# Performance work log

Measured on AMD Instinct MI355X. Metric: run time of the kernel, lower is better.

Reference implementation:

```python
import jax, jax.numpy as jnp
import numpy as np

INPUT_SIZE = 512
LABEL_NUM = 8
OUTPUT_SIZE = 64
H1 = 1024  # shared bottom width
H2 = 512   # expert hidden width
B = 8192


def setup_inputs() -> dict:
    key = jax.random.key(0)
    ks = jax.random.split(key, 8)
    s_in = 1.0 / np.sqrt(INPUT_SIZE)
    s_h1 = 1.0 / np.sqrt(H1)
    s_h2 = 1.0 / np.sqrt(H2)
    return {
        "input": jax.random.normal(ks[0], (B, INPUT_SIZE), dtype=jnp.float32),
        "category": jax.random.randint(ks[1], (B,), 0, LABEL_NUM, dtype=jnp.int32),
        # shared bottom Linear(input_size, 1024): stored as [in, out]
        "W_in": jax.random.uniform(ks[2], (INPUT_SIZE, H1), jnp.float32, -s_in, s_in),
        "b_in": jax.random.uniform(ks[3], (H1,), jnp.float32, -s_in, s_in),
        # per-expert Linear(1024, 512) stacked over experts
        "W1": jax.random.uniform(ks[4], (LABEL_NUM, H1, H2), jnp.float32, -s_h1, s_h1),
        "b1": jax.random.uniform(ks[5], (LABEL_NUM, H2), jnp.float32, -s_h1, s_h1),
        # per-expert Linear(512, output_size) stacked over experts
        "W2": jax.random.uniform(ks[6], (LABEL_NUM, H2, OUTPUT_SIZE), jnp.float32, -s_h2, s_h2),
        "b2": jax.random.uniform(ks[7], (LABEL_NUM, OUTPUT_SIZE), jnp.float32, -s_h2, s_h2),
    }


def reference(input, category, W_in, b_in, W1, b1, W2, b2):
    # Shared bottom: Linear + ELU -> [B, H1]
    mid = jax.nn.elu(input @ W_in + b_in)
    # Run all experts densely, then hard-select per-sample expert output.
    # (Faithful to per-sample hard routing; small expert count makes this clean.)
    h = jax.nn.elu(jnp.einsum("bd,edh->beh", mid, W1) + b1[None, :, :])  # [B,E,H2]
    out_all = jnp.einsum("beh,eho->beo", h, W2) + b2[None, :, :]          # [B,E,O]
    # gather the chosen expert's output for each sample
    out = jnp.take_along_axis(out_all, category[:, None, None].astype(jnp.int32).repeat(1, axis=1), axis=1)
    return out[:, 0, :]  # [B, O]
```

## Files before the change

### kernel.cpp

```cpp
#include <hip/hip_runtime.h>

typedef unsigned short u16;
typedef unsigned int u32;
typedef __bf16 bf16x8 __attribute__((ext_vector_type(8)));
typedef float f32x4 __attribute__((ext_vector_type(4)));

#define GLD_LDS(gptr, lptr) \
  __builtin_amdgcn_global_load_lds((const __attribute__((address_space(1))) void*)(gptr), \
                                   (__attribute__((address_space(3))) void*)(lptr), 16, 0, 0)

__device__ __forceinline__ u16 f2b(float f) {
  union { __bf16 h; u16 u; } v; v.h = (__bf16)f; return v.u;
}
__device__ __forceinline__ float elu1(float v) {
  return v > 0.f ? v : (__expf(v) - 1.f);
}

__device__ void transpose_tile(float (*tbuf)[65], const float* __restrict__ src,
                               u16* __restrict__ dst, int R, int C, int tr, int tc,
                               size_t zoff) {
  const int tid = threadIdx.x;
  const float* sp = src + zoff + (size_t)(tr * 64) * C + tc * 64;
#pragma unroll
  for (int i = 0; i < 4; i++) {
    const int rr = (tid >> 4) + i * 16, f = tid & 15;
    float4 v = *reinterpret_cast<const float4*>(sp + (size_t)rr * C + f * 4);
    tbuf[rr][f * 4 + 0] = v.x; tbuf[rr][f * 4 + 1] = v.y;
    tbuf[rr][f * 4 + 2] = v.z; tbuf[rr][f * 4 + 3] = v.w;
  }
  __syncthreads();
  u16* dp = dst + zoff + (size_t)(tc * 64) * R + tr * 64;
#pragma unroll
  for (int i = 0; i < 4; i++) {
    const int u = tid + i * 256;
    const int c = u >> 4, rq = u & 15;
    ushort4 w;
    w.x = f2b(tbuf[rq * 4 + 0][c]); w.y = f2b(tbuf[rq * 4 + 1][c]);
    w.z = f2b(tbuf[rq * 4 + 2][c]); w.w = f2b(tbuf[rq * 4 + 3][c]);
    *reinterpret_cast<ushort4*>(dp + (size_t)c * R + rq * 4) = w;
  }
}

__device__ void hist_body(int rb, const int* __restrict__ cat, int* __restrict__ cnts) {
  __shared__ int c8[8];
  const int tid = threadIdx.x;
  if (tid < 8) c8[tid] = 0;
  __syncthreads();
  if (tid < 128) atomicAdd(&c8[cat[rb * 128 + tid]], 1);
  __syncthreads();
  if (tid < 8) cnts[rb * 8 + tid] = c8[tid];
}

__device__ void scatter_body(int rb, const int* __restrict__ cat,
                             const int* __restrict__ cnts,
                             int* __restrict__ list, int* __restrict__ off) {
  __shared__ int lc[512];
  __shared__ int lcur[8];
  __shared__ int starts[8];
  const int tid = threadIdx.x;
  lc[tid] = cnts[tid];
  lc[tid + 256] = cnts[tid + 256];
  if (tid < 8) lcur[tid] = 0;
  __syncthreads();
  if (tid < 8) {
    const int c = tid;
    int base = 0;
    for (int cc = 0; cc < c; cc++) {
      int s = 0;
      for (int b = 0; b < 64; b++) s += lc[b * 8 + cc];
      base += s;
    }
    int pre = 0;
    for (int b = 0; b < rb; b++) pre += lc[b * 8 + c];
    starts[c] = base + pre;
    if (rb == 0) {
      off[c] = base;
      if (c == 7) {
        int s = 0;
        for (int b = 0; b < 64; b++) s += lc[b * 8 + 7];
        off[8] = base + s;
      }
    }
  }
  __syncthreads();
  if (tid < 128) {
    const int idx = rb * 128 + tid;
    const int c = cat[idx];
    const int r = atomicAdd(&lcur[c], 1);
    list[starts[c] + r] = idx;
  }
}

__global__ __launch_bounds__(256) void wsmall(const float* __restrict__ W_in,
                                              const int* __restrict__ cat,
                                              u16* __restrict__ o0, int* __restrict__ cnts) {
  __shared__ float tbuf[64][65];
  if (blockIdx.x >= 128) { hist_body(blockIdx.x - 128, cat, cnts); return; }
  transpose_tile(tbuf, W_in, o0, 512, 1024, blockIdx.x >> 4, blockIdx.x & 15, 0);
}


template<int LAYER, int BN, int K, int N>
__global__ __launch_bounds__(256, 4) void gemm_t(
    const float* __restrict__ Xf, const u16* __restrict__ A,
    const u16* __restrict__ Bw, const float* __restrict__ bias,
    const int* __restrict__ list, const int* __restrict__ off,
    u16* __restrict__ outb, float* __restrict__ outf,
    const int* __restrict__ cat, const int* __restrict__ cnts,
    int* __restrict__ wlist, int* __restrict__ woff,
    const float* __restrict__ Wc1, const float* __restrict__ Wc2,
    u16* __restrict__ o1, u16* __restrict__ o2) {
  struct GBuf { alignas(16) u16 As[2][2048]; alignas(16) u16 Bs[2][BN * 32]; };
  __shared__ union SM { GBuf g; float tbuf[64][65]; } sm;

  const int tid = threadIdx.x;

  if constexpr (LAYER == 1) {
    if (blockIdx.y == 8) {
      if (blockIdx.x < 64) scatter_body(blockIdx.x, cat, cnts, wlist, woff);
      return;
    }
    if (blockIdx.y >= 9) {
      if (blockIdx.y <= 16) {
        const int t = (blockIdx.y - 9) * 128 + blockIdx.x;
        const int z = t >> 7, rem = t & 127;
        transpose_tile(sm.tbuf, Wc1, o1, 1024, 512, rem >> 3, rem & 7,
                       (size_t)z * 1024 * 512);
      } else if (blockIdx.x < 64) {
        const int t = blockIdx.x, z = t >> 3;
        transpose_tile(sm.tbuf, Wc2, o2, 512, 64, t & 7, 0, (size_t)z * 512 * 64);
      }
      return;
    }
  }

  int tidx, col0;
  if constexpr (LAYER == 1) {
    const int orig = blockIdx.y * 128 + blockIdx.x;
    const int work = (orig & 7) * 128 + (orig >> 3);
    tidx = work >> 3;
    col0 = (work & 7) * BN;
  } else if constexpr (LAYER == 2) {
    const int orig = blockIdx.y * 136 + blockIdx.x;
    const int work = (orig & 7) * 68 + (orig >> 3);
    tidx = work >> 2;
    col0 = (work & 3) * BN;
  } else {
    const int orig = blockIdx.x;
    const int work = (orig & 7) * 17 + (orig >> 3);
    tidx = work;
    col0 = 0;
  }

  const int wave = tid >> 6, lane = tid & 63;

  int e = 0, start = 0, cnt = 0, rowbase;
  if constexpr (LAYER == 1) {
    rowbase = tidx * 64;
  } else {
    int t = tidx;
    int found = -1;
    for (e = 0; e < 8; e++) {
      int tiles = (off[e + 1] - off[e] + 63) >> 6;
      if (t < tiles) { found = e; break; }
      t -= tiles;
    }
    if (found < 0) return;
    start = off[e];
    cnt = off[e + 1] - start;
    rowbase = t * 64;
  }

  const int srow = tid >> 2, skc = tid & 3;
  const int kxs = (skc ^ (srow & 3)) * 8;

  const float* ax = nullptr;
  const u16* a_src = nullptr;
  if constexpr (LAYER == 1) {
    ax = Xf + (size_t)(rowbase + srow) * K + kxs;
  } else if constexpr (LAYER == 2) {
    int gr = list[start + min(rowbase + srow, cnt - 1)];
    a_src = A + (size_t)gr * K + kxs;
  } else {
    a_src = A + (size_t)(start + min(rowbase + srow, cnt - 1)) * K + kxs;
  }
  const u16* Bbase = Bw + (LAYER == 1 ? (size_t)0 : (size_t)e * N * K);
  const u16* b_src0 = Bbase + (size_t)(col0 + srow) * K + kxs;
  const u16* b_src1 = Bbase + (size_t)(col0 + 64 + srow) * K + kxs;

  const int wbase = wave * 512;

  constexpr int NR = BN / 32;
  const int wy = wave & 1, wx = wave >> 1;
  const int fr = lane & 15, kg = lane >> 4;
  const int kx = (kg ^ (fr & 3)) * 8;
  const int ar0 = (wy * 32 + fr) * 32 + kx;
  const int br0 = (wx * (BN / 2) + fr) * 32 + kx;

  f32x4 acc[2][NR] = {};

  float4 va0, va1;
  auto LOAD_A1 = [&](int t) {
    va0 = *reinterpret_cast<const float4*>(ax + t * 32);
    va1 = *reinterpret_cast<const float4*>(ax + t * 32 + 4);
  };
  auto WRITE_A1 = [&](int buf) {
    uint4 w;
    w.x = (u32)f2b(va0.x) | ((u32)f2b(va0.y) << 16);
    w.y = (u32)f2b(va0.z) | ((u32)f2b(va0.w) << 16);
    w.z = (u32)f2b(va1.x) | ((u32)f2b(va1.y) << 16);
    w.w = (u32)f2b(va1.z) | ((u32)f2b(va1.w) << 16);
    *reinterpret_cast<uint4*>(&sm.g.As[buf][srow * 32 + skc * 8]) = w;
  };
  auto COMPUTE = [&](int buf) {
    bf16x8 af[2], bfv[NR];
#pragma unroll
    for (int m = 0; m < 2; m++) af[m] = *(const bf16x8*)&sm.g.As[buf][ar0 + m * 16 * 32];
#pragma unroll
    for (int n = 0; n < NR; n++) bfv[n] = *(const bf16x8*)&sm.g.Bs[buf][br0 + n * 16 * 32];
#pragma unroll
    for (int m = 0; m < 2; m++)
#pragma unroll
      for (int n = 0; n < NR; n++)
        acc[m][n] = __builtin_amdgcn_mfma_f32_16x16x32_bf16(af[m], bfv[n], acc[m][n], 0, 0, 0);
  };

  constexpr int NK = K / 32;
  if constexpr (LAYER == 1) LOAD_A1(0);
  else GLD_LDS(a_src, &sm.g.As[0][wbase]);
  GLD_LDS(b_src0, &sm.g.Bs[0][wbase]);
  if constexpr (BN == 128) GLD_LDS(b_src1, &sm.g.Bs[0][2048 + wbase]);
  if constexpr (LAYER == 1) WRITE_A1(0);
  __syncthreads();

  for (int it = 0; it < NK; ++it) {
    const int cur = it & 1;
    const int nxt = cur ^ 1;
    if (it + 1 < NK) {
      const int kt = (it + 1) * 32;
      if constexpr (LAYER == 1) LOAD_A1(it + 1);
      else GLD_LDS(a_src + kt, &sm.g.As[nxt][wbase]);
      GLD_LDS(b_src0 + kt, &sm.g.Bs[nxt][wbase]);
      if constexpr (BN == 128) GLD_LDS(b_src1 + kt, &sm.g.Bs[nxt][2048 + wbase]);
    }
    COMPUTE(cur);
    if constexpr (LAYER == 1) { if (it + 1 < NK) WRITE_A1(nxt); }
    __syncthreads();
  }

#pragma unroll
  for (int n = 0; n < NR; n++) {
    const int col = col0 + wx * (BN / 2) + n * 16 + fr;
    const float bc = bias[(LAYER == 1 ? 0 : e * N) + col];
#pragma unroll
    for (int m = 0; m < 2; m++) {
      const int rloc = wy * 32 + m * 16 + kg * 4;
#pragma unroll
      for (int j = 0; j < 4; j++) {
        const float v = acc[m][n][j] + bc;
        if constexpr (LAYER == 1) {
          outb[(size_t)(rowbase + rloc + j) * N + col] = f2b(elu1(v));
        } else if constexpr (LAYER == 2) {
          const int slot = rowbase + rloc + j;
          if (slot < cnt) outb[(size_t)(start + slot) * N + col] = f2b(elu1(v));
        } else {
          const int slot = rowbase + rloc + j;
          if (slot < cnt) outf[(size_t)list[start + slot] * N + col] = v;
        }
      }
    }
  }
}


extern "C" void kernel_launch(void* const* d_in, const int* in_sizes, int n_in,
                              void* d_out, int out_size, void* d_ws, size_t ws_size,
                              hipStream_t stream) {
  const float* x    = (const float*)d_in[0];
  const int*   cat  = (const int*)d_in[1];
  const float* W_in = (const float*)d_in[2];
  const float* b_in = (const float*)d_in[3];
  const float* W1   = (const float*)d_in[4];
  const float* b1   = (const float*)d_in[5];
  const float* W2   = (const float*)d_in[6];
  const float* b2   = (const float*)d_in[7];
  float* out = (float*)d_out;

  char* p = (char*)d_ws;
  u16* midb = (u16*)p; p += (size_t)8192 * 1024 * 2;
  u16* hb   = (u16*)p; p += (size_t)8192 * 512 * 2;
  u16* wtin = (u16*)p; p += (size_t)1024 * 512 * 2;
  u16* w1t  = (u16*)p; p += (size_t)8 * 512 * 1024 * 2;
  u16* w2t  = (u16*)p; p += (size_t)8 * 64 * 512 * 2;
  int* list = (int*)p; p += (size_t)8192 * 4;
  int* off  = (int*)p; p += 64;
  int* cnts = (int*)p; p += 64 * 8 * 4;

  wsmall<<<192, 256, 0, stream>>>(W_in, cat, wtin, cnts);

  gemm_t<1, 128, 512, 1024><<<dim3(128, 18), 256, 0, stream>>>(
      x, nullptr, wtin, b_in, nullptr, nullptr, midb, nullptr,
      cat, cnts, list, off, W1, W2, w1t, w2t);

  gemm_t<2, 128, 1024, 512><<<dim3(136, 4), 256, 0, stream>>>(
      nullptr, midb, w1t, b1, list, off, hb, nullptr,
      nullptr, nullptr, nullptr, nullptr, nullptr, nullptr, nullptr, nullptr);

  gemm_t<3, 64, 512, 64><<<dim3(136, 1), 256, 0, stream>>>(
      nullptr, hb, w2t, b2, list, off, nullptr, out,
      nullptr, nullptr, nullptr, nullptr, nullptr, nullptr, nullptr, nullptr);
}
```

Measured before the change: 64.33 us.

## Triple-buffer LDS pipeline with partial vmcnt waits for expert GEMM layers

For layers 2 and 3, the GEMM main loop now uses three LDS buffers with async global-to-LDS loads issued two k-steps ahead. Each step waits only on the older loads via a partial s_waitcnt vmcnt, then a single barrier, replacing the full-drain double-buffer scheme. This is meant to hide global memory latency better and remove one barrier per iteration. It raises LDS usage for those layers, which may reduce occupancy, and it relies on the count of outstanding loads per stage being exactly right.

```diff
diff --git a/kernel.cpp b/kernel.cpp
--- a/kernel.cpp
+++ b/kernel.cpp
@@ -110,7 +110,8 @@
     int* __restrict__ wlist, int* __restrict__ woff,
     const float* __restrict__ Wc1, const float* __restrict__ Wc2,
     u16* __restrict__ o1, u16* __restrict__ o2) {
-  struct GBuf { alignas(16) u16 As[2][2048]; alignas(16) u16 Bs[2][BN * 32]; };
+  constexpr int NBUF = (LAYER == 1) ? 2 : 3;
+  struct GBuf { alignas(16) u16 As[NBUF][2048]; alignas(16) u16 Bs[NBUF][BN * 32]; };
   __shared__ union SM { GBuf g; float tbuf[64][65]; } sm;
 
   const int tid = threadIdx.x;
@@ -212,6 +213,12 @@
     w.w = (u32)f2b(va1.z) | ((u32)f2b(va1.w) << 16);
     *reinterpret_cast<uint4*>(&sm.g.As[buf][srow * 32 + skc * 8]) = w;
   };
+  auto STAGE = [&](int t, int buf) {
+    const int kt = t * 32;
+    GLD_LDS(a_src + kt, &sm.g.As[buf][wbase]);
+    GLD_LDS(b_src0 + kt, &sm.g.Bs[buf][wbase]);
+    if constexpr (BN == 128) GLD_LDS(b_src1 + kt, &sm.g.Bs[buf][2048 + wbase]);
+  };
   auto COMPUTE = [&](int buf) {
     bf16x8 af[2], bfv[NR];
 #pragma unroll
@@ -226,26 +233,41 @@
   };
 
   constexpr int NK = K / 32;
-  if constexpr (LAYER == 1) LOAD_A1(0);
-  else GLD_LDS(a_src, &sm.g.As[0][wbase]);
-  GLD_LDS(b_src0, &sm.g.Bs[0][wbase]);
-  if constexpr (BN == 128) GLD_LDS(b_src1, &sm.g.Bs[0][2048 + wbase]);
-  if constexpr (LAYER == 1) WRITE_A1(0);
-  __syncthreads();
-
-  for (int it = 0; it < NK; ++it) {
-    const int cur = it & 1;
-    const int nxt = cur ^ 1;
-    if (it + 1 < NK) {
-      const int kt = (it + 1) * 32;
-      if constexpr (LAYER == 1) LOAD_A1(it + 1);
-      else GLD_LDS(a_src + kt, &sm.g.As[nxt][wbase]);
-      GLD_LDS(b_src0 + kt, &sm.g.Bs[nxt][wbase]);
-      if constexpr (BN == 128) GLD_LDS(b_src1 + kt, &sm.g.Bs[nxt][2048 + wbase]);
-    }
-    COMPUTE(cur);
-    if constexpr (LAYER == 1) { if (it + 1 < NK) WRITE_A1(nxt); }
+
+  if constexpr (LAYER == 1) {
+    LOAD_A1(0);
+    GLD_LDS(b_src0, &sm.g.Bs[0][wbase]);
+    if constexpr (BN == 128) GLD_LDS(b_src1, &sm.g.Bs[0][2048 + wbase]);
+    WRITE_A1(0);
     __syncthreads();
+    for (int it = 0; it < NK; ++it) {
+      const int cur = it & 1;
+      const int nxt = cur ^ 1;
+      if (it + 1 < NK) {
+        const int kt = (it + 1) * 32;
+        LOAD_A1(it + 1);
+        GLD_LDS(b_src0 + kt, &sm.g.Bs[nxt][wbase]);
+        if constexpr (BN == 128) GLD_LDS(b_src1 + kt, &sm.g.Bs[nxt][2048 + wbase]);
+      }
+      COMPUTE(cur);
+      if (it + 1 < NK) WRITE_A1(nxt);
+      __syncthreads();
+    }
+  } else {
+    constexpr int S = (BN == 128) ? 3 : 2;
+    STAGE(0, 0);
+    STAGE(1, 1);
+    int b0 = 0, b1 = 1, b2 = 2;
+    for (int t = 0; t < NK - 1; ++t) {
+      asm volatile("s_waitcnt vmcnt(%0)" :: "n"(S) : "memory");
+      __builtin_amdgcn_s_barrier();
+      if (t + 2 < NK) STAGE(t + 2, b2);
+      COMPUTE(b0);
+      const int tmp = b0; b0 = b1; b1 = b2; b2 = tmp;
+    }
+    asm volatile("s_waitcnt vmcnt(0)" ::: "memory");
+    __builtin_amdgcn_s_barrier();
+    COMPUTE(b0);
   }
 
 #pragma unroll
```

Measured after the change: 65.21 us. About the same (+1.4%).

## Fuse expert second layer into first expert GEMM with atomic split-K output

Applied to the files above, without the earlier changes.

Removes the separate third GEMM kernel and the hb intermediate buffer. Each layer-2 block stages its 64x128 ELU tile in LDS and multiplies it by the matching 128-row slice of the W2 expert weights. The partial 64-wide outputs are accumulated into the final output with float atomics, and the output is pre-initialised with the per-sample b2 bias in the first small kernel. This saves a launch and the round trip of h through global memory, at the cost of four atomic adds per output element and a nondeterministic summation order.

```diff
diff --git a/kernel.cpp b/kernel.cpp
--- a/kernel.cpp
+++ b/kernel.cpp
@@ -93,10 +93,23 @@
 
 __global__ __launch_bounds__(256) void wsmall(const float* __restrict__ W_in,
                                               const int* __restrict__ cat,
-                                              u16* __restrict__ o0, int* __restrict__ cnts) {
+                                              const float* __restrict__ b2,
+                                              u16* __restrict__ o0, int* __restrict__ cnts,
+                                              float* __restrict__ out) {
   __shared__ float tbuf[64][65];
-  if (blockIdx.x >= 128) { hist_body(blockIdx.x - 128, cat, cnts); return; }
-  transpose_tile(tbuf, W_in, o0, 512, 1024, blockIdx.x >> 4, blockIdx.x & 15, 0);
+  const int bid = blockIdx.x, tid = threadIdx.x;
+  if (bid >= 192) {
+    const int r = (bid - 192) * 32 + (tid >> 3);
+    const int co = (tid & 7) * 8;
+    const int c = cat[r];
+    float4 v0 = *reinterpret_cast<const float4*>(b2 + c * 64 + co);
+    float4 v1 = *reinterpret_cast<const float4*>(b2 + c * 64 + co + 4);
+    *reinterpret_cast<float4*>(out + (size_t)r * 64 + co) = v0;
+    *reinterpret_cast<float4*>(out + (size_t)r * 64 + co + 4) = v1;
+    return;
+  }
+  if (bid >= 128) { hist_body(bid - 128, cat, cnts); return; }
+  transpose_tile(tbuf, W_in, o0, 512, 1024, bid >> 4, bid & 15, 0);
 }
 
 
@@ -111,7 +124,11 @@
     const float* __restrict__ Wc1, const float* __restrict__ Wc2,
     u16* __restrict__ o1, u16* __restrict__ o2) {
   struct GBuf { alignas(16) u16 As[2][2048]; alignas(16) u16 Bs[2][BN * 32]; };
-  __shared__ union SM { GBuf g; float tbuf[64][65]; } sm;
+  __shared__ union SM {
+    GBuf g;
+    float tbuf[64][65];
+    u16 ht[64 * 136];
+  } sm;
 
   const int tid = threadIdx.x;
 
@@ -140,16 +157,11 @@
     const int work = (orig & 7) * 128 + (orig >> 3);
     tidx = work >> 3;
     col0 = (work & 7) * BN;
-  } else if constexpr (LAYER == 2) {
+  } else {
     const int orig = blockIdx.y * 136 + blockIdx.x;
     const int work = (orig & 7) * 68 + (orig >> 3);
     tidx = work >> 2;
     col0 = (work & 3) * BN;
-  } else {
-    const int orig = blockIdx.x;
-    const int work = (orig & 7) * 17 + (orig >> 3);
-    tidx = work;
-    col0 = 0;
   }
 
   const int wave = tid >> 6, lane = tid & 63;
@@ -178,11 +190,9 @@
   const u16* a_src = nullptr;
   if constexpr (LAYER == 1) {
     ax = Xf + (size_t)(rowbase + srow) * K + kxs;
-  } else if constexpr (LAYER == 2) {
+  } else {
     int gr = list[start + min(rowbase + srow, cnt - 1)];
     a_src = A + (size_t)gr * K + kxs;
-  } else {
-    a_src = A + (size_t)(start + min(rowbase + srow, cnt - 1)) * K + kxs;
   }
   const u16* Bbase = Bw + (LAYER == 1 ? (size_t)0 : (size_t)e * N * K);
   const u16* b_src0 = Bbase + (size_t)(col0 + srow) * K + kxs;
@@ -248,24 +258,62 @@
     __syncthreads();
   }
 
-#pragma unroll
-  for (int n = 0; n < NR; n++) {
-    const int col = col0 + wx * (BN / 2) + n * 16 + fr;
-    const float bc = bias[(LAYER == 1 ? 0 : e * N) + col];
-#pragma unroll
-    for (int m = 0; m < 2; m++) {
-      const int rloc = wy * 32 + m * 16 + kg * 4;
-#pragma unroll
-      for (int j = 0; j < 4; j++) {
-        const float v = acc[m][n][j] + bc;
-        if constexpr (LAYER == 1) {
-          outb[(size_t)(rowbase + rloc + j) * N + col] = f2b(elu1(v));
-        } else if constexpr (LAYER == 2) {
-          const int slot = rowbase + rloc + j;
-          if (slot < cnt) outb[(size_t)(start + slot) * N + col] = f2b(elu1(v));
-        } else {
-          const int slot = rowbase + rloc + j;
-          if (slot < cnt) outf[(size_t)list[start + slot] * N + col] = v;
+  if constexpr (LAYER == 1) {
+#pragma unroll
+    for (int n = 0; n < NR; n++) {
+      const int col = col0 + wx * (BN / 2) + n * 16 + fr;
+      const float bc = bias[col];
+#pragma unroll
+      for (int m = 0; m < 2; m++) {
+        const int rloc = wy * 32 + m * 16 + kg * 4;
+#pragma unroll
+        for (int j = 0; j < 4; j++)
+          outb[(size_t)(rowbase + rloc + j) * N + col] = f2b(elu1(acc[m][n][j] + bc));
+      }
+    }
+  } else {
+#pragma unroll
+    for (int n = 0; n < NR; n++) {
+      const int lcol = wx * 64 + n * 16 + fr;
+      const float bc = bias[e * N + col0 + lcol];
+#pragma unroll
+      for (int m = 0; m < 2; m++) {
+        const int rl = wy * 32 + m * 16 + kg * 4;
+#pragma unroll
+        for (int j = 0; j < 4; j++)
+          sm.ht[(rl + j) * 136 + lcol] = f2b(elu1(acc[m][n][j] + bc));
+      }
+    }
+    __syncthreads();
+
+    const u16* w2p = o2 + (size_t)e * 64 * 512 + col0;
+    f32x4 po[2][2] = {};
+#pragma unroll
+    for (int ks = 0; ks < 4; ks++) {
+      bf16x8 pa[2], pb[2];
+#pragma unroll
+      for (int m = 0; m < 2; m++)
+        pa[m] = *(const bf16x8*)&sm.ht[(wy * 32 + m * 16 + fr) * 136 + ks * 32 + kg * 8];
+#pragma unroll
+      for (int n = 0; n < 2; n++)
+        pb[n] = *(const bf16x8*)&w2p[(size_t)(wx * 32 + n * 16 + fr) * 512 + ks * 32 + kg * 8];
+#pragma unroll
+      for (int m = 0; m < 2; m++)
+#pragma unroll
+        for (int n = 0; n < 2; n++)
+          po[m][n] = __builtin_amdgcn_mfma_f32_16x16x32_bf16(pa[m], pb[n], po[m][n], 0, 0, 0);
+    }
+#pragma unroll
+    for (int n = 0; n < 2; n++) {
+      const int oc = wx * 32 + n * 16 + fr;
+#pragma unroll
+      for (int m = 0; m < 2; m++) {
+        const int sl0 = rowbase + wy * 32 + m * 16 + kg * 4;
+#pragma unroll
+        for (int j = 0; j < 4; j++) {
+          const int slot = sl0 + j;
+          if (slot < cnt)
+            atomicAdd(&outf[(size_t)list[start + slot] * 64 + oc], po[m][n][j]);
         }
       }
     }
@@ -288,7 +336,6 @@
 
   char* p = (char*)d_ws;
   u16* midb = (u16*)p; p += (size_t)8192 * 1024 * 2;
-  u16* hb   = (u16*)p; p += (size_t)8192 * 512 * 2;
   u16* wtin = (u16*)p; p += (size_t)1024 * 512 * 2;
   u16* w1t  = (u16*)p; p += (size_t)8 * 512 * 1024 * 2;
   u16* w2t  = (u16*)p; p += (size_t)8 * 64 * 512 * 2;
@@ -296,17 +343,13 @@
   int* off  = (int*)p; p += 64;
   int* cnts = (int*)p; p += 64 * 8 * 4;
 
-  wsmall<<<192, 256, 0, stream>>>(W_in, cat, wtin, cnts);
+  wsmall<<<448, 256, 0, stream>>>(W_in, cat, b2, wtin, cnts, out);
 
   gemm_t<1, 128, 512, 1024><<<dim3(128, 18), 256, 0, stream>>>(
       x, nullptr, wtin, b_in, nullptr, nullptr, midb, nullptr,
       cat, cnts, list, off, W1, W2, w1t, w2t);
 
   gemm_t<2, 128, 1024, 512><<<dim3(136, 4), 256, 0, stream>>>(
-      nullptr, midb, w1t, b1, list, off, hb, nullptr,
-      nullptr, nullptr, nullptr, nullptr, nullptr, nullptr, nullptr, nullptr);
-
-  gemm_t<3, 64, 512, 64><<<dim3(136, 1), 256, 0, stream>>>(
-      nullptr, hb, w2t, b2, list, off, nullptr, out,
-      nullptr, nullptr, nullptr, nullptr, nullptr, nullptr, nullptr, nullptr);
-}
+      nullptr, midb, w1t, b1, list, off, nullptr, out,
+      nullptr, nullptr, nullptr, nullptr, nullptr, nullptr, nullptr, w2t);
+}
```

New measurement: 59.73 us. -7.1%, faster.
